# Kernel optimization log

Measured on AMD Instinct MI355X. Metric: run time of the kernel, lower is better.

Reference implementation:

```python
import jax, jax.numpy as jnp
import numpy as np

WH, WW = 16, 16            # window size
NUM_HEADS = 8


def _relative_position_index(wh, ww):
    ch = jnp.arange(wh)
    cw = jnp.arange(ww)
    coords = jnp.stack(jnp.meshgrid(ch, cw, indexing='ij'))        # [2, wh, ww]
    coords = coords.reshape(2, -1)                                  # [2, N]
    rel = coords[:, :, None] - coords[:, None, :]                   # [2, N, N]
    rel = rel.transpose(1, 2, 0)                                    # [N, N, 2]
    idx = (rel[..., 0] + wh - 1) * (2 * ww - 1) + (rel[..., 1] + ww - 1)
    return idx                                                      # [N, N] int32


def setup_inputs() -> dict:
    key = jax.random.key(0)
    ks = jax.random.split(key, 7)
    B, N, C = 128, WH * WW, 512
    x = jax.random.normal(ks[0], (B, N, C), dtype=jnp.float32)
    y = jax.random.normal(ks[1], (B, N, C), dtype=jnp.float32)
    # Linear weights stored as [in, out]; init ~ standard scale
    q_w = jax.random.normal(ks[2], (C, C), dtype=jnp.float32) * (C ** -0.5)
    kv_w = jax.random.normal(ks[3], (C, 2 * C), dtype=jnp.float32) * (C ** -0.5)
    proj_w = jax.random.normal(ks[4], (C, C), dtype=jnp.float32) * (C ** -0.5)
    proj_b = jax.random.normal(ks[5], (C,), dtype=jnp.float32) * 0.01
    n_rel = (2 * WH - 1) * (2 * WW - 1)  # 961
    bias_table = jax.random.normal(ks[6], (n_rel, NUM_HEADS), dtype=jnp.float32) * 0.02
    return {"x": x, "y": y, "q_w": q_w, "kv_w": kv_w,
            "proj_w": proj_w, "proj_b": proj_b, "bias_table": bias_table}


def reference(x, y, q_w, kv_w, proj_w, proj_b, bias_table):
    B, N1, C = x.shape
    _, N2, _ = y.shape
    H = NUM_HEADS
    d = C // H
    scale = d ** -0.5

    q = (x @ q_w).reshape(B, N1, H, d).transpose(0, 2, 1, 3)        # [B,H,N1,d]
    kv = (y @ kv_w).reshape(B, N2, 2, H, d)
    k = kv[:, :, 0].transpose(0, 2, 1, 3)                           # [B,H,N2,d]
    v = kv[:, :, 1].transpose(0, 2, 1, 3)                           # [B,H,N2,d]

    attn = jnp.einsum('bhqd,bhkd->bhqk', q, k) * scale              # [B,H,N1,N2]

    idx = _relative_position_index(WH, WW)                          # [N, N]
    rel_bias = bias_table[idx.reshape(-1)].reshape(N1, N2, H)       # gather
    rel_bias = rel_bias.transpose(2, 0, 1)                          # [H,N1,N2]
    attn = attn + rel_bias[None]

    attn = jax.nn.softmax(attn, axis=-1)
    out = jnp.einsum('bhqk,bhkd->bhqd', attn, v)                    # [B,H,N1,d]
    out = out.transpose(0, 2, 1, 3).reshape(B, N1, C)
    out = out @ proj_w + proj_b
    return out
```

## Files before the change

kernel.cpp:

```cpp
#include <hip/hip_runtime.h>

typedef unsigned short u16;
typedef __attribute__((ext_vector_type(8))) short short8;
typedef __attribute__((ext_vector_type(4))) float floatx4;
typedef __attribute__((ext_vector_type(4))) unsigned short ushort4v;

__device__ __forceinline__ float bf2f(u16 v){
  union { unsigned int u; float f; } x; x.u = ((unsigned int)v) << 16; return x.f;
}
__device__ __forceinline__ u16 f2bf(float f){
  union { float f; unsigned int u; } x; x.f = f;
  unsigned int r = x.u + 0x7FFFu + ((x.u >> 16) & 1u);
  return (u16)(r >> 16);
}
__device__ __forceinline__ short8 cvt8(float4 f0, float4 f1){
  short8 v;
  v[0] = (short)f2bf(f0.x); v[1] = (short)f2bf(f0.y);
  v[2] = (short)f2bf(f0.z); v[3] = (short)f2bf(f0.w);
  v[4] = (short)f2bf(f1.x); v[5] = (short)f2bf(f1.y);
  v[6] = (short)f2bf(f1.z); v[7] = (short)f2bf(f1.w);
  return v;
}

__device__ __forceinline__ void async16(const void* g, void* l){
  __builtin_amdgcn_global_load_lds(
      (__attribute__((address_space(1))) unsigned int*)const_cast<void*>(g),
      (__attribute__((address_space(3))) unsigned int*)l, 16, 0, 0);
}

__global__ __launch_bounds__(256)
void conv_bf16(const float* __restrict__ in, u16* __restrict__ out, int n8){
  const int stride = gridDim.x * 256;
  for (int i = blockIdx.x * 256 + threadIdx.x; i < n8; i += stride){
    float4 f0 = ((const float4*)in)[(size_t)i * 2];
    float4 f1 = ((const float4*)in)[(size_t)i * 2 + 1];
    *(short8*)(out + (size_t)i * 8) = cvt8(f0, f1);
  }
}

__global__ void transpose_f32(const float* __restrict__ in, u16* __restrict__ out,
                              int R, int C){
  __shared__ u16 t[32][33];
  const int tx = threadIdx.x;
  const int c0 = blockIdx.x * 32, r0 = blockIdx.y * 32;
  for (int i = tx; i < 1024; i += 256){
    int r = i >> 5, c = i & 31;
    t[r][c] = f2bf(in[(size_t)(r0 + r) * C + c0 + c]);
  }
  __syncthreads();
  for (int i = tx; i < 1024; i += 256){
    int r = i >> 5, c = i & 31;
    out[(size_t)(c0 + r) * R + r0 + c] = t[c][r];
  }
}

__global__ void bias_expand(const float* __restrict__ table, u16* __restrict__ Bm){
  int i = blockIdx.x * 256 + threadIdx.x;
  int k = i >> 8, q = i & 255;
  int rh = (q >> 4) - (k >> 4) + 15;
  int rw = (q & 15) - (k & 15) + 15;
  int idx = rh * 31 + rw;
  #pragma unroll
  for (int h = 0; h < 8; h++)
    Bm[h * 65536 + i] = f2bf(8.0f * table[(size_t)idx * 8 + h]);
}

template<int MODE, int GX>
__global__ __launch_bounds__(512, 2)
void gemm_bt(const u16* __restrict__ A, const u16* __restrict__ Bt,
             void* __restrict__ O0, u16* __restrict__ O1,
             const float* __restrict__ bias)
{
  __shared__ __align__(16) u16 As[3][256 * 64];
  __shared__ __align__(16) u16 Bs[3][128 * 64];
  const int tid  = threadIdx.x;
  const int lane = tid & 63, wave = tid >> 6;
  const int q16  = lane & 15, quad = lane >> 4;
  const int wr   = wave >> 1, wc = wave & 1;

  constexpr int NWG = 128 * GX;
  constexpr int CPX = NWG / 8;
  const int bid = blockIdx.x;
  const int swz = (bid & 7) * CPX + (bid >> 3);
  const int rowBase = (swz / GX) * 256;
  const int colBase = (swz % GX) * 128;

  const u16* Ap = A  + (size_t)rowBase * 512;
  const u16* Bp = Bt + (size_t)colBase * 512;

  floatx4 acc[4][4];
  #pragma unroll
  for (int i = 0; i < 4; i++)
    #pragma unroll
    for (int j = 0; j < 4; j++) acc[i][j] = floatx4{0.f, 0.f, 0.f, 0.f};

  int sra[4], sca[4];
  #pragma unroll
  for (int j = 0; j < 4; j++){
    int p = tid + j * 512;
    sra[j] = p >> 3;
    sca[j] = ((p & 7) ^ (sra[j] & 7)) * 8;
  }

  auto STAGE = [&](int slot, int kt){
    #pragma unroll
    for (int j = 0; j < 4; j++){
      u16* d = &As[slot][(size_t)(j * 512 + wave * 64) * 8];
      async16(Ap + (size_t)sra[j] * 512 + kt * 64 + sca[j], d);
    }
    #pragma unroll
    for (int j = 0; j < 2; j++){
      u16* d = &Bs[slot][(size_t)(j * 512 + wave * 64) * 8];
      async16(Bp + (size_t)sra[j] * 512 + kt * 64 + sca[j], d);
    }
  };

  STAGE(0, 0);
  STAGE(1, 1);

  #pragma unroll
  for (int kt = 0; kt < 8; kt++){
    const int cs = kt % 3;
    if (kt < 7) asm volatile("s_waitcnt vmcnt(6)" ::: "memory");
    else        asm volatile("s_waitcnt vmcnt(0)" ::: "memory");
    __builtin_amdgcn_s_barrier();
    __builtin_amdgcn_sched_barrier(0);
    if (kt + 2 < 8) STAGE((kt + 2) % 3, kt + 2);
    __builtin_amdgcn_sched_barrier(0);

    __builtin_amdgcn_s_setprio(1);
    #pragma unroll
    for (int kk = 0; kk < 2; kk++){
      short8 af[4], bfr[4];
      #pragma unroll
      for (int mt = 0; mt < 4; mt++){
        int r  = wr * 64 + mt * 16 + q16;
        int ph = ((kk * 4 + quad) ^ (r & 7)) * 8;
        af[mt] = *(const short8*)(&As[cs][r * 64 + ph]);
      }
      #pragma unroll
      for (int nt = 0; nt < 4; nt++){
        int r  = wc * 64 + nt * 16 + q16;
        int ph = ((kk * 4 + quad) ^ (r & 7)) * 8;
        bfr[nt] = *(const short8*)(&Bs[cs][r * 64 + ph]);
      }
      #pragma unroll
      for (int mt = 0; mt < 4; mt++)
        #pragma unroll
        for (int nt = 0; nt < 4; nt++)
          acc[mt][nt] = __builtin_amdgcn_mfma_f32_16x16x32_bf16(
              af[mt], bfr[nt], acc[mt][nt], 0, 0, 0);
    }
    __builtin_amdgcn_s_setprio(0);
  }

  #pragma unroll
  for (int mt = 0; mt < 4; mt++){
    #pragma unroll
    for (int nt = 0; nt < 4; nt++){
      const floatx4 v = acc[mt][nt];
      const int col = colBase + wc * 64 + nt * 16 + q16;
      #pragma unroll
      for (int r = 0; r < 4; r++){
        const int row = rowBase + wr * 64 + mt * 16 + quad * 4 + r;
        if (MODE == 0){
          int bb = row >> 8, n = row & 255, hh = col >> 6, dd = col & 63;
          ((u16*)O0)[(((size_t)(bb * 8 + hh)) * 256 + n) * 64 + dd] = f2bf(v[r]);
        } else if (MODE == 1){
          int bb = row >> 8, key = row & 255;
          int two = col >> 9, hh = (col >> 6) & 7, dd = col & 63;
          if (two == 0)
            ((u16*)O0)[(((size_t)(bb * 8 + hh)) * 256 + key) * 64 + dd] = f2bf(v[r]);
          else
            O1[(((size_t)(bb * 8 + hh)) * 64 + dd) * 256 + key] = f2bf(v[r]);
        } else {
          ((float*)O0)[(size_t)row * 512 + col] = v[r] + bias[col];
        }
      }
    }
  }
}

__global__ __launch_bounds__(512)
void attn_kernel(const u16* __restrict__ Qb, const u16* __restrict__ Kb,
                 const u16* __restrict__ Vtb, const u16* __restrict__ Bm,
                 u16* __restrict__ Ob)
{
  constexpr int PS = 264;
  __shared__ __align__(16) u16 Ks[256 * 64];
  __shared__ __align__(16) u16 Vs[64 * 256];
  __shared__ __align__(16) u16 Pss[8 * 16 * PS];
  const int bh = blockIdx.x;
  const int b = bh >> 3, h = bh & 7;
  const u16* Qp = Qb  + (size_t)bh * 256 * 64;
  const u16* Kp = Kb  + (size_t)bh * 256 * 64;
  const u16* Vp = Vtb + (size_t)bh * 64 * 256;
  const u16* Bp = Bm  + (size_t)h * 65536;
  const int tid = threadIdx.x;
  const int lane = tid & 63, wave = tid >> 6;
  const int q16 = lane & 15, quad = lane >> 4;
  u16* Pw = Pss + wave * 16 * PS;

  #pragma unroll
  for (int j = 0; j < 4; j++){
    int g = tid + j * 512;
    int row = g >> 3, phys = g & 7;
    async16(Kp + row * 64 + ((phys ^ (row & 7)) * 8),
            &Ks[(size_t)(j * 512 + wave * 64) * 8]);
  }
  #pragma unroll
  for (int j = 0; j < 4; j++){
    int g = tid + j * 512;
    int row = g >> 5, phys = g & 31;
    async16(Vp + row * 256 + ((phys ^ (row & 7)) * 8),
            &Vs[(size_t)(j * 512 + wave * 64) * 8]);
  }
  asm volatile("s_waitcnt vmcnt(4)" ::: "memory");
  __builtin_amdgcn_s_barrier();

  for (int chunk = 0; chunk < 2; chunk++){
    const int qbase = wave * 32 + chunk * 16;
    const short8 qa0 = *(const short8*)(Qp + (qbase + q16) * 64 + quad * 8);
    const short8 qa1 = *(const short8*)(Qp + (qbase + q16) * 64 + 32 + quad * 8);

    floatx4 acc[16];
    #pragma unroll
    for (int kt = 0; kt < 16; kt++){
      ushort4v bv = *(const ushort4v*)(Bp + (size_t)(kt * 16 + q16) * 256
                                          + qbase + quad * 4);
      floatx4 a;
      a[0] = bf2f(bv[0]); a[1] = bf2f(bv[1]);
      a[2] = bf2f(bv[2]); a[3] = bf2f(bv[3]);
      acc[kt] = a;
    }

    __builtin_amdgcn_s_setprio(1);
    #pragma unroll
    for (int kt = 0; kt < 16; kt++){
      const int row = kt * 16 + q16;
      const short8 k0 = *(const short8*)(&Ks[row * 64 + ((quad       ^ (row & 7)) * 8)]);
      const short8 k1 = *(const short8*)(&Ks[row * 64 + (((quad + 4) ^ (row & 7)) * 8)]);
      acc[kt] = __builtin_amdgcn_mfma_f32_16x16x32_bf16(qa0, k0, acc[kt], 0, 0, 0);
      acc[kt] = __builtin_amdgcn_mfma_f32_16x16x32_bf16(qa1, k1, acc[kt], 0, 0, 0);
    }
    __builtin_amdgcn_s_setprio(0);

    floatx4 mrow = {-3e38f, -3e38f, -3e38f, -3e38f};
    #pragma unroll
    for (int kt = 0; kt < 16; kt++){
      #pragma unroll
      for (int r = 0; r < 4; r++) mrow[r] = fmaxf(mrow[r], acc[kt][r]);
    }
    #pragma unroll
    for (int off = 1; off < 16; off <<= 1){
      #pragma unroll
      for (int r = 0; r < 4; r++)
        mrow[r] = fmaxf(mrow[r], __shfl_xor(mrow[r], off, 64));
    }

    const float Cf = 0.125f * 1.4426950408889634f;
    floatx4 lrow = {0.f, 0.f, 0.f, 0.f};
    #pragma unroll
    for (int kt = 0; kt < 16; kt++){
      #pragma unroll
      for (int r = 0; r < 4; r++){
        float e = exp2f((acc[kt][r] - mrow[r]) * Cf);
        lrow[r] += e;
        Pw[(quad * 4 + r) * PS + kt * 16 + q16] = f2bf(e);
      }
    }
    #pragma unroll
    for (int off = 1; off < 16; off <<= 1){
      #pragma unroll
      for (int r = 0; r < 4; r++) lrow[r] += __shfl_xor(lrow[r], off, 64);
    }

    if (chunk == 0){
      asm volatile("s_waitcnt vmcnt(0)" ::: "memory");
      __builtin_amdgcn_s_barrier();
    }

    floatx4 o[4];
    #pragma unroll
    for (int nt = 0; nt < 4; nt++) o[nt] = floatx4{0.f, 0.f, 0.f, 0.f};
    #pragma unroll
    for (int half = 0; half < 2; half++){
      short8 pa[4];
      #pragma unroll
      for (int k2 = 0; k2 < 4; k2++)
        pa[k2] = *(const short8*)(Pw + q16 * PS + (half * 4 + k2) * 32 + quad * 8);
      __builtin_amdgcn_s_setprio(1);
      #pragma unroll
      for (int nt = 0; nt < 4; nt++)
        #pragma unroll
        for (int k2 = 0; k2 < 4; k2++){
          const int row = nt * 16 + q16;
          const int c32 = (half * 4 + k2) * 4 + quad;
          const short8 vb = *(const short8*)(&Vs[row * 256 + ((c32 ^ (row & 7)) * 8)]);
          o[nt] = __builtin_amdgcn_mfma_f32_16x16x32_bf16(pa[k2], vb, o[nt], 0, 0, 0);
        }
      __builtin_amdgcn_s_setprio(0);
    }

    floatx4 rl;
    #pragma unroll
    for (int r = 0; r < 4; r++) rl[r] = 1.0f / lrow[r];
    #pragma unroll
    for (int nt = 0; nt < 4; nt++)
      #pragma unroll
      for (int r = 0; r < 4; r++){
        int q = qbase + quad * 4 + r;
        Ob[((size_t)(b * 256 + q)) * 512 + h * 64 + nt * 16 + q16] =
            f2bf(o[nt][r] * rl[r]);
      }
  }
}

extern "C" void kernel_launch(void* const* d_in, const int* in_sizes, int n_in,
                              void* d_out, int out_size, void* d_ws, size_t ws_size,
                              hipStream_t stream)
{
  (void)in_sizes; (void)n_in; (void)out_size; (void)ws_size;
  const float* x      = (const float*)d_in[0];
  const float* y      = (const float*)d_in[1];
  const float* q_w    = (const float*)d_in[2];
  const float* kv_w   = (const float*)d_in[3];
  const float* proj_w = (const float*)d_in[4];
  const float* proj_b = (const float*)d_in[5];
  const float* btab   = (const float*)d_in[6];
  float* out = (float*)d_out;
  char* w = (char*)d_ws;

  u16* Qb   = (u16*)(w);
  u16* Kb   = (u16*)(w + 33554432);
  u16* Vtb  = (u16*)(w + 67108864);
  u16* Ab   = (u16*)(w + 100663296);
  u16* qwT  = (u16*)(w + 134217728);
  u16* kvwT = (u16*)(w + 134742016);
  u16* pwT  = (u16*)(w + 135790592);
  u16* Bm   = (u16*)(w + 136314880);

  transpose_f32<<<dim3(16, 16), 256, 0, stream>>>(q_w,    qwT,  512, 512);
  transpose_f32<<<dim3(32, 16), 256, 0, stream>>>(kv_w,   kvwT, 512, 1024);
  transpose_f32<<<dim3(16, 16), 256, 0, stream>>>(proj_w, pwT,  512, 512);
  bias_expand<<<dim3(256), 256, 0, stream>>>(btab, Bm);

  conv_bf16<<<dim3(2048), 256, 0, stream>>>(x, Ab, 2097152);
  gemm_bt<0, 4><<<dim3(512),  512, 0, stream>>>(Ab, qwT,  Qb,  nullptr, nullptr);
  conv_bf16<<<dim3(2048), 256, 0, stream>>>(y, Ab, 2097152);
  gemm_bt<1, 8><<<dim3(1024), 512, 0, stream>>>(Ab, kvwT, Kb,  Vtb,     nullptr);
  attn_kernel<<<dim3(1024), 512, 0, stream>>>(Qb, Kb, Vtb, Bm, Ab);
  gemm_bt<2, 4><<<dim3(512),  512, 0, stream>>>(Ab, pwT,  out, nullptr, proj_b);
}
```

Baseline: 400.9 us.

## Compute transposed QK^T so softmax probabilities stay in registers, dropping LDS staging

Swaps the MFMA operand order so each lane holds one query row's scores across keys. The row max and sum then need only two cross-lane shuffles, and the bias matrix layout is transposed to match. Probabilities are packed to bf16 with v_cvt_pk_bf16_f32 and regrouped into the PV A-operand through register shuffles, so the shared-memory P buffer and its write/read round trip are gone. This frees LDS and removes bank traffic, at the cost of more ds_bpermute shuffles and selects per k-step.

```diff
diff --git a/kernel.cpp b/kernel.cpp
--- a/kernel.cpp
+++ b/kernel.cpp
@@ -56,7 +56,7 @@
 
 __global__ void bias_expand(const float* __restrict__ table, u16* __restrict__ Bm){
   int i = blockIdx.x * 256 + threadIdx.x;
-  int k = i >> 8, q = i & 255;
+  int q = i >> 8, k = i & 255;
   int rh = (q >> 4) - (k >> 4) + 15;
   int rw = (q & 15) - (k & 15) + 15;
   int idx = rh * 31 + rw;
@@ -186,10 +186,8 @@
                  const u16* __restrict__ Vtb, const u16* __restrict__ Bm,
                  u16* __restrict__ Ob)
 {
-  constexpr int PS = 264;
   __shared__ __align__(16) u16 Ks[256 * 64];
   __shared__ __align__(16) u16 Vs[64 * 256];
-  __shared__ __align__(16) u16 Pss[8 * 16 * PS];
   const int bh = blockIdx.x;
   const int b = bh >> 3, h = bh & 7;
   const u16* Qp = Qb  + (size_t)bh * 256 * 64;
@@ -199,7 +197,6 @@
   const int tid = threadIdx.x;
   const int lane = tid & 63, wave = tid >> 6;
   const int q16 = lane & 15, quad = lane >> 4;
-  u16* Pw = Pss + wave * 16 * PS;
 
   #pragma unroll
   for (int j = 0; j < 4; j++){
@@ -218,16 +215,20 @@
   asm volatile("s_waitcnt vmcnt(4)" ::: "memory");
   __builtin_amdgcn_s_barrier();
 
+  const int la = q16 + ((quad & 1) << 5);
+  const int lb = la + 16;
+  const bool hi = (quad >> 1) != 0;
+
   for (int chunk = 0; chunk < 2; chunk++){
     const int qbase = wave * 32 + chunk * 16;
-    const short8 qa0 = *(const short8*)(Qp + (qbase + q16) * 64 + quad * 8);
-    const short8 qa1 = *(const short8*)(Qp + (qbase + q16) * 64 + 32 + quad * 8);
+    const int qrow  = qbase + q16;
+    const short8 qa0 = *(const short8*)(Qp + qrow * 64 + quad * 8);
+    const short8 qa1 = *(const short8*)(Qp + qrow * 64 + 32 + quad * 8);
 
     floatx4 acc[16];
     #pragma unroll
     for (int kt = 0; kt < 16; kt++){
-      ushort4v bv = *(const ushort4v*)(Bp + (size_t)(kt * 16 + q16) * 256
-                                          + qbase + quad * 4);
+      ushort4v bv = *(const ushort4v*)(Bp + (size_t)qrow * 256 + kt * 16 + quad * 4);
       floatx4 a;
       a[0] = bf2f(bv[0]); a[1] = bf2f(bv[1]);
       a[2] = bf2f(bv[2]); a[3] = bf2f(bv[3]);
@@ -240,40 +241,40 @@
       const int row = kt * 16 + q16;
       const short8 k0 = *(const short8*)(&Ks[row * 64 + ((quad       ^ (row & 7)) * 8)]);
       const short8 k1 = *(const short8*)(&Ks[row * 64 + (((quad + 4) ^ (row & 7)) * 8)]);
-      acc[kt] = __builtin_amdgcn_mfma_f32_16x16x32_bf16(qa0, k0, acc[kt], 0, 0, 0);
-      acc[kt] = __builtin_amdgcn_mfma_f32_16x16x32_bf16(qa1, k1, acc[kt], 0, 0, 0);
+      acc[kt] = __builtin_amdgcn_mfma_f32_16x16x32_bf16(k0, qa0, acc[kt], 0, 0, 0);
+      acc[kt] = __builtin_amdgcn_mfma_f32_16x16x32_bf16(k1, qa1, acc[kt], 0, 0, 0);
     }
     __builtin_amdgcn_s_setprio(0);
 
-    floatx4 mrow = {-3e38f, -3e38f, -3e38f, -3e38f};
+    floatx4 m4 = acc[0];
+    #pragma unroll
+    for (int kt = 1; kt < 16; kt++){
+      m4[0] = fmaxf(m4[0], acc[kt][0]);
+      m4[1] = fmaxf(m4[1], acc[kt][1]);
+      m4[2] = fmaxf(m4[2], acc[kt][2]);
+      m4[3] = fmaxf(m4[3], acc[kt][3]);
+    }
+    float m = fmaxf(fmaxf(m4[0], m4[1]), fmaxf(m4[2], m4[3]));
+    m = fmaxf(m, __shfl_xor(m, 16, 64));
+    m = fmaxf(m, __shfl_xor(m, 32, 64));
+
+    const float Cf = 0.125f * 1.4426950408889634f;
+    unsigned int w[32];
+    floatx4 l4 = {0.f, 0.f, 0.f, 0.f};
     #pragma unroll
     for (int kt = 0; kt < 16; kt++){
-      #pragma unroll
-      for (int r = 0; r < 4; r++) mrow[r] = fmaxf(mrow[r], acc[kt][r]);
-    }
-    #pragma unroll
-    for (int off = 1; off < 16; off <<= 1){
-      #pragma unroll
-      for (int r = 0; r < 4; r++)
-        mrow[r] = fmaxf(mrow[r], __shfl_xor(mrow[r], off, 64));
-    }
-
-    const float Cf = 0.125f * 1.4426950408889634f;
-    floatx4 lrow = {0.f, 0.f, 0.f, 0.f};
-    #pragma unroll
-    for (int kt = 0; kt < 16; kt++){
-      #pragma unroll
-      for (int r = 0; r < 4; r++){
-        float e = exp2f((acc[kt][r] - mrow[r]) * Cf);
-        lrow[r] += e;
-        Pw[(quad * 4 + r) * PS + kt * 16 + q16] = f2bf(e);
-      }
-    }
-    #pragma unroll
-    for (int off = 1; off < 16; off <<= 1){
-      #pragma unroll
-      for (int r = 0; r < 4; r++) lrow[r] += __shfl_xor(lrow[r], off, 64);
-    }
+      float e0 = exp2f((acc[kt][0] - m) * Cf);
+      float e1 = exp2f((acc[kt][1] - m) * Cf);
+      float e2 = exp2f((acc[kt][2] - m) * Cf);
+      float e3 = exp2f((acc[kt][3] - m) * Cf);
+      l4[0] += e0; l4[1] += e1; l4[2] += e2; l4[3] += e3;
+      asm("v_cvt_pk_bf16_f32 %0, %1, %2" : "=v"(w[2 * kt])     : "v"(e0), "v"(e1));
+      asm("v_cvt_pk_bf16_f32 %0, %1, %2" : "=v"(w[2 * kt + 1]) : "v"(e2), "v"(e3));
+    }
+    float l = (l4[0] + l4[1]) + (l4[2] + l4[3]);
+    l += __shfl_xor(l, 16, 64);
+    l += __shfl_xor(l, 32, 64);
+    const float rl = 1.0f / l;
 
     if (chunk == 0){
       asm volatile("s_waitcnt vmcnt(0)" ::: "memory");
@@ -284,34 +285,41 @@
     #pragma unroll
     for (int nt = 0; nt < 4; nt++) o[nt] = floatx4{0.f, 0.f, 0.f, 0.f};
     #pragma unroll
-    for (int half = 0; half < 2; half++){
-      short8 pa[4];
-      #pragma unroll
-      for (int k2 = 0; k2 < 4; k2++)
-        pa[k2] = *(const short8*)(Pw + q16 * PS + (half * 4 + k2) * 32 + quad * 8);
+    for (int s = 0; s < 8; s++){
+      int a0 = __shfl((int)w[4 * s + 0], la, 64);
+      int a1 = __shfl((int)w[4 * s + 1], la, 64);
+      int A0 = __shfl((int)w[4 * s + 2], la, 64);
+      int A1 = __shfl((int)w[4 * s + 3], la, 64);
+      int b0 = __shfl((int)w[4 * s + 0], lb, 64);
+      int b1 = __shfl((int)w[4 * s + 1], lb, 64);
+      int B0 = __shfl((int)w[4 * s + 2], lb, 64);
+      int B1 = __shfl((int)w[4 * s + 3], lb, 64);
+      union { int u[4]; short8 s8; } P;
+      P.u[0] = hi ? A0 : a0;
+      P.u[1] = hi ? A1 : a1;
+      P.u[2] = hi ? B0 : b0;
+      P.u[3] = hi ? B1 : b1;
       __builtin_amdgcn_s_setprio(1);
       #pragma unroll
-      for (int nt = 0; nt < 4; nt++)
-        #pragma unroll
-        for (int k2 = 0; k2 < 4; k2++){
-          const int row = nt * 16 + q16;
-          const int c32 = (half * 4 + k2) * 4 + quad;
-          const short8 vb = *(const short8*)(&Vs[row * 256 + ((c32 ^ (row & 7)) * 8)]);
-          o[nt] = __builtin_amdgcn_mfma_f32_16x16x32_bf16(pa[k2], vb, o[nt], 0, 0, 0);
-        }
+      for (int nt = 0; nt < 4; nt++){
+        const int row = nt * 16 + q16;
+        const int c32 = s * 4 + quad;
+        const short8 vb = *(const short8*)(&Vs[row * 256 + ((c32 ^ (row & 7)) * 8)]);
+        o[nt] = __builtin_amdgcn_mfma_f32_16x16x32_bf16(P.s8, vb, o[nt], 0, 0, 0);
+      }
       __builtin_amdgcn_s_setprio(0);
     }
 
-    floatx4 rl;
-    #pragma unroll
-    for (int r = 0; r < 4; r++) rl[r] = 1.0f / lrow[r];
+    float rlr[4];
+    #pragma unroll
+    for (int r = 0; r < 4; r++) rlr[r] = __shfl(rl, quad * 4 + r, 64);
     #pragma unroll
     for (int nt = 0; nt < 4; nt++)
       #pragma unroll
       for (int r = 0; r < 4; r++){
         int q = qbase + quad * 4 + r;
         Ob[((size_t)(b * 256 + q)) * 512 + h * 64 + nt * 16 + q16] =
-            f2bf(o[nt][r] * rl[r]);
+            f2bf(o[nt][r] * rlr[r]);
       }
   }
 }
```

After: 389.3 us. -2.9%, faster.
